# Performance work log

Measured on AMD Instinct MI355X. Metric: run time of the kernel, lower is better.

Reference implementation:

```python
import jax, jax.numpy as jnp
import numpy as np

D_MODEL = 1024
N_HEADS = 16
HEAD_DIM = D_MODEL // N_HEADS
WINDOW = 256
N_GLOBAL = 2
EPS = 1e-5


def _layernorm(x, g, b):
    mu = jnp.mean(x, axis=-1, keepdims=True)
    var = jnp.var(x, axis=-1, keepdims=True)
    return (x - mu) * jax.lax.rsqrt(var + EPS) * g + b


def _longformer_mask(T):
    i = jnp.arange(T)[:, None]
    j = jnp.arange(T)[None, :]
    half = WINDOW // 2
    local = (j >= i - half) & (j <= i + half)
    glob = jnp.zeros((T, T), dtype=bool)
    if N_GLOBAL >= 1:
        glob = glob | (i == 0) | (j == 0)
    if N_GLOBAL >= 2 and T > 1:
        glob = glob | (i == T - 1) | (j == T - 1)
    allowed = (local | glob) & (j <= i)  # causal
    neg_inf = jnp.float32(-jnp.inf)
    return jnp.where(allowed, jnp.float32(0.0), neg_inf)[None, None]  # (1,1,T,T)


def setup_inputs() -> dict:
    key = jax.random.key(0)
    ks = jax.random.split(key, 8)
    B, T, D = 2, 2048, D_MODEL
    s = 0.02
    return {
        "x": jax.random.normal(ks[0], (B, T, D), dtype=jnp.float32),
        "ln1_g": jnp.ones((D,), jnp.float32),
        "ln1_b": jnp.zeros((D,), jnp.float32),
        "ln2_g": jnp.ones((D,), jnp.float32),
        "ln2_b": jnp.zeros((D,), jnp.float32),
        "Wq": jax.random.normal(ks[1], (D, D), jnp.float32) * s,
        "Wk": jax.random.normal(ks[2], (D, D), jnp.float32) * s,
        "Wv": jax.random.normal(ks[3], (D, D), jnp.float32) * s,
        "Wo": jax.random.normal(ks[4], (D, D), jnp.float32) * s,
        "bo": jnp.zeros((D,), jnp.float32),
        "W1": jax.random.normal(ks[5], (D, 4 * D), jnp.float32) * s,
        "b1": jnp.zeros((4 * D,), jnp.float32),
        "W2": jax.random.normal(ks[6], (4 * D, D), jnp.float32) * s,
        "b2": jnp.zeros((D,), jnp.float32),
    }


def reference(x, ln1_g, ln1_b, ln2_g, ln2_b, Wq, Wk, Wv, Wo, bo, W1, b1, W2, b2):
    B, T, D = x.shape
    h = _layernorm(x, ln1_g, ln1_b)
    # (B,T,D) -> (B,H,T,hd)
    q = (h @ Wq).reshape(B, T, N_HEADS, HEAD_DIM).transpose(0, 2, 1, 3)
    k = (h @ Wk).reshape(B, T, N_HEADS, HEAD_DIM).transpose(0, 2, 1, 3)
    v = (h @ Wv).reshape(B, T, N_HEADS, HEAD_DIM).transpose(0, 2, 1, 3)
    mask = _longformer_mask(T)
    scores = jnp.einsum("bhqd,bhkd->bhqk", q, k) / np.sqrt(HEAD_DIM) + mask
    attn = jax.nn.softmax(scores, axis=-1)
    out = jnp.einsum("bhqk,bhkd->bhqd", attn, v)
    out = out.transpose(0, 2, 1, 3).reshape(B, T, D)
    x = x + out @ Wo + bo
    h2 = _layernorm(x, ln2_g, ln2_b)
    ffn = jax.nn.gelu(h2 @ W1 + b1, approximate=False) @ W2 + b2
    return x + ffn
```

## Files before the change

### kernel.cpp

```cpp
#include <hip/hip_runtime.h>
#include <cmath>

#define Tseq 2048
#define Dm   1024
#define NHd  16
#define HDim 64
#define Mrows 4096
#define QS   3072
#define PAD  72
#define NSPLIT 16

typedef _Float16 f16;
typedef _Float16 half8 __attribute__((ext_vector_type(8)));
typedef _Float16 half4 __attribute__((ext_vector_type(4)));
typedef float    floatx4 __attribute__((ext_vector_type(4)));

#define ASYNC_COPY16(g, l)                                                       \
  __builtin_amdgcn_global_load_lds((const __attribute__((address_space(1))) void*)(g), \
                                   (__attribute__((address_space(3))) void*)(l), 16, 0, 0)

__device__ __forceinline__ float gelu_f(float v) {
  const float u = 0.7978845608028654f * (v + 0.044715f * v * v * v);
  const float e = __expf(2.0f * u);
  return 0.5f * v * (2.0f - 2.0f / (e + 1.0f));
}

__global__ __launch_bounds__(256) void transp_f16(const float* __restrict__ W,
                                                  f16* __restrict__ Wt, int K, int N) {
  __shared__ float tile[32][33];
  const int n0 = blockIdx.x * 32, k0 = blockIdx.y * 32;
  const int tx = threadIdx.x & 31, ty = threadIdx.x >> 5;
#pragma unroll
  for (int i = 0; i < 32; i += 8)
    tile[ty + i][tx] = W[(size_t)(k0 + ty + i) * N + n0 + tx];
  __syncthreads();
#pragma unroll
  for (int i = 0; i < 32; i += 8)
    Wt[(size_t)(n0 + ty + i) * K + k0 + tx] = (f16)tile[tx][ty + i];
}

__global__ __launch_bounds__(256) void transp_qkv(const float* __restrict__ Wq,
                                                  const float* __restrict__ Wk,
                                                  const float* __restrict__ Wv,
                                                  f16* __restrict__ Wt) {
  __shared__ float tile[32][33];
  const float* W = (blockIdx.z == 0) ? Wq : (blockIdx.z == 1) ? Wk : Wv;
  f16* dst = Wt + (size_t)blockIdx.z * Dm * Dm;
  const int n0 = blockIdx.x * 32, k0 = blockIdx.y * 32;
  const int tx = threadIdx.x & 31, ty = threadIdx.x >> 5;
#pragma unroll
  for (int i = 0; i < 32; i += 8)
    tile[ty + i][tx] = W[(size_t)(k0 + ty + i) * Dm + n0 + tx];
  __syncthreads();
#pragma unroll
  for (int i = 0; i < 32; i += 8)
    dst[(size_t)(n0 + ty + i) * Dm + k0 + tx] = (f16)tile[tx][ty + i];
}

__global__ __launch_bounds__(256) void ln_f16(const float* __restrict__ x,
                                              const float* __restrict__ g,
                                              const float* __restrict__ bb,
                                              f16* __restrict__ out) {
  const int row = blockIdx.x, t = threadIdx.x;
  const float4 v = ((const float4*)(x + (size_t)row * Dm))[t];
  float s  = v.x + v.y + v.z + v.w;
  float ss = v.x * v.x + v.y * v.y + v.z * v.z + v.w * v.w;
#pragma unroll
  for (int m = 32; m >= 1; m >>= 1) { s += __shfl_xor(s, m); ss += __shfl_xor(ss, m); }
  __shared__ float red[8];
  if ((t & 63) == 0) { red[t >> 6] = s; red[4 + (t >> 6)] = ss; }
  __syncthreads();
  const float S  = red[0] + red[1] + red[2] + red[3];
  const float SS = red[4] + red[5] + red[6] + red[7];
  const float mean = S * (1.0f / Dm);
  const float inv  = rsqrtf(SS * (1.0f / Dm) - mean * mean + 1e-5f);
  const float4 gg = ((const float4*)g)[t];
  const float4 bv = ((const float4*)bb)[t];
  half4 o;
  o.x = (f16)(((v.x - mean) * inv) * gg.x + bv.x);
  o.y = (f16)(((v.y - mean) * inv) * gg.y + bv.y);
  o.z = (f16)(((v.z - mean) * inv) * gg.z + bv.z);
  o.w = (f16)(((v.w - mean) * inv) * gg.w + bv.w);
  *((half4*)(out + (size_t)row * Dm) + t) = o;
}

template <int NS>
__global__ __launch_bounds__(256) void reduce_ln(const f16* __restrict__ P,
                                                 const float* __restrict__ resid,
                                                 const float* __restrict__ bias,
                                                 const float* __restrict__ g,
                                                 const float* __restrict__ bb,
                                                 float* __restrict__ x1,
                                                 f16* __restrict__ h) {
  const int row = blockIdx.x, t = threadIdx.x;
  const size_t idx = (size_t)row * (Dm / 4) + t;
  const float4 r = ((const float4*)resid)[idx];
  const float4 b = ((const float4*)bias)[t];
  float4 o; o.x = r.x + b.x; o.y = r.y + b.y; o.z = r.z + b.z; o.w = r.w + b.w;
#pragma unroll
  for (int z = 0; z < NS; ++z) {
    const half4 p = ((const half4*)(P + (size_t)z * Mrows * Dm))[idx];
    o.x += (float)p[0]; o.y += (float)p[1]; o.z += (float)p[2]; o.w += (float)p[3];
  }
  ((float4*)x1)[idx] = o;
  float s  = o.x + o.y + o.z + o.w;
  float ss = o.x * o.x + o.y * o.y + o.z * o.z + o.w * o.w;
#pragma unroll
  for (int m = 32; m >= 1; m >>= 1) { s += __shfl_xor(s, m); ss += __shfl_xor(ss, m); }
  __shared__ float red[8];
  if ((t & 63) == 0) { red[t >> 6] = s; red[4 + (t >> 6)] = ss; }
  __syncthreads();
  const float S  = red[0] + red[1] + red[2] + red[3];
  const float SS = red[4] + red[5] + red[6] + red[7];
  const float mean = S * (1.0f / Dm);
  const float inv  = rsqrtf(SS * (1.0f / Dm) - mean * mean + 1e-5f);
  const float4 gg = ((const float4*)g)[t];
  const float4 bv = ((const float4*)bb)[t];
  half4 oh;
  oh[0] = (f16)(((o.x - mean) * inv) * gg.x + bv.x);
  oh[1] = (f16)(((o.y - mean) * inv) * gg.y + bv.y);
  oh[2] = (f16)(((o.z - mean) * inv) * gg.z + bv.z);
  oh[3] = (f16)(((o.w - mean) * inv) * gg.w + bv.w);
  ((half4*)h)[idx] = oh;
}

template <int NS>
__global__ __launch_bounds__(256) void reduceK(const f16* __restrict__ P,
                                               const float* __restrict__ resid,
                                               const float* __restrict__ bias,
                                               float* __restrict__ out) {
  const int t = blockIdx.x * 256 + threadIdx.x;
  const int col4 = t & (Dm / 4 - 1);
  const float4 r = ((const float4*)resid)[t];
  const float4 b = ((const float4*)bias)[col4];
  float4 o; o.x = r.x + b.x; o.y = r.y + b.y; o.z = r.z + b.z; o.w = r.w + b.w;
#pragma unroll
  for (int z = 0; z < NS; ++z) {
    const half4 p = ((const half4*)(P + (size_t)z * Mrows * Dm))[t];
    o.x += (float)p[0]; o.y += (float)p[1]; o.z += (float)p[2]; o.w += (float)p[3];
  }
  ((float4*)out)[t] = o;
}

template <int EPI, int LNZ>
__global__ __launch_bounds__(256, 4) void gemm_f16(const f16* __restrict__ A,
                                                   const f16* __restrict__ Bt,
                                                   int M, int N, int K, int kLen,
                                                   const float* __restrict__ bias,
                                                   f16* __restrict__ Ch) {
  constexpr int NZ = 1 << LNZ;
  __shared__ f16 As[128 * 64];
  __shared__ f16 Bs[128 * 64];
  const int tid = threadIdx.x;
  int bx, by, bz;
  if (EPI == 5) {
    const int lin = blockIdx.x;
    bz = lin & (NZ - 1);
    bx = (lin >> LNZ) & 7;
    by = lin >> (LNZ + 3);
  } else {
    bx = blockIdx.x; by = blockIdx.y; bz = 0;
  }
  const int m0 = by * 128, n0 = bx * 128;
  const int kOff = bz * kLen;
  const int w = tid >> 6, l = tid & 63;
  const int wr = (w >> 1) * 64, wc = (w & 1) * 64;
  const int c = l & 15, qq = l >> 4;
  const int cx = c & 7;
  const int srow = tid >> 3;
  const int scol = ((tid & 7) ^ (srow & 7)) * 8;

  floatx4 acc[4][4] = {};

  const f16* Ab = A + (size_t)(m0 + srow) * K + kOff + scol;
  const f16* Bb = Bt + (size_t)(n0 + srow) * K + kOff + scol;

  for (int k0 = 0; k0 < kLen; k0 += 64) {
    __syncthreads();
#pragma unroll
    for (int i = 0; i < 4; ++i) {
      ASYNC_COPY16(Ab + k0 + (size_t)(i * 32) * K, As + i * 2048 + w * 512);
      ASYNC_COPY16(Bb + k0 + (size_t)(i * 32) * K, Bs + i * 2048 + w * 512);
    }
    __syncthreads();
    half8 af[4][2], bfr[4][2];
#pragma unroll
    for (int t = 0; t < 4; ++t) {
      const int ra = (wr + t * 16 + c) * 64;
      af[t][0] = *(const half8*)&As[ra + ((qq ^ cx) * 8)];
      af[t][1] = *(const half8*)&As[ra + (((4 + qq) ^ cx) * 8)];
      const int rb = (wc + t * 16 + c) * 64;
      bfr[t][0] = *(const half8*)&Bs[rb + ((qq ^ cx) * 8)];
      bfr[t][1] = *(const half8*)&Bs[rb + (((4 + qq) ^ cx) * 8)];
    }
#pragma unroll
    for (int ti = 0; ti < 4; ++ti)
#pragma unroll
      for (int tj = 0; tj < 4; ++tj) {
        acc[ti][tj] = __builtin_amdgcn_mfma_f32_16x16x32_f16(af[ti][0], bfr[tj][0], acc[ti][tj], 0, 0, 0);
        acc[ti][tj] = __builtin_amdgcn_mfma_f32_16x16x32_f16(af[ti][1], bfr[tj][1], acc[ti][tj], 0, 0, 0);
      }
  }

  f16* Cw = (EPI == 5) ? (Ch + (size_t)bz * M * N) : Ch;
#pragma unroll
  for (int ti = 0; ti < 4; ++ti)
#pragma unroll
    for (int tj = 0; tj < 4; ++tj)
#pragma unroll
      for (int r = 0; r < 4; ++r) {
        const int row = m0 + wr + ti * 16 + qq * 4 + r;
        const int col = n0 + wc + tj * 16 + c;
        const size_t idx = (size_t)row * N + col;
        float v = acc[ti][tj][r];
        if (EPI == 2) {
          Cw[idx] = (f16)gelu_f(v + bias[col]);
        } else {
          Cw[idx] = (f16)v;
        }
      }
}

__global__ __launch_bounds__(256, 4) void attn_win(const f16* __restrict__ qkv,
                                                   f16* __restrict__ ao) {
  __shared__ f16 qs[64 * PAD];
  __shared__ f16 ks[64 * PAD];
  __shared__ f16 vts[64 * PAD];
  __shared__ f16 ps[64 * PAD];
  const int qt = blockIdx.x;
  const int b = blockIdx.y >> 4, hh = blockIdx.y & 15;
  const int q0 = qt * 64;
  const int tid = threadIdx.x, w = tid >> 6, l = tid & 63;
  const int c = l & 15, qq = l >> 4;
  const int wr = w * 16;
  const size_t base = ((size_t)b * Tseq) * QS + hh * HDim;
  const int rr = tid >> 2, ss = (tid & 3) * 16;

  {
    const f16* src = qkv + base + (size_t)(q0 + rr) * QS + ss;
    *(uint4*)&qs[rr * PAD + ss]     = *(const uint4*)src;
    *(uint4*)&qs[rr * PAD + ss + 8] = *(const uint4*)(src + 8);
  }

  float m_run[4], l_run[4];
  floatx4 oacc[4];
#pragma unroll
  for (int r = 0; r < 4; ++r) { m_run[r] = -INFINITY; l_run[r] = 0.f; }
#pragma unroll
  for (int td = 0; td < 4; ++td) oacc[td] = (floatx4){0.f, 0.f, 0.f, 0.f};

  int chunks[4]; int nch = 0;
  if (qt > 2) chunks[nch++] = 0;
  for (int ch = (qt - 2 > 0 ? qt - 2 : 0); ch <= qt; ++ch) chunks[nch++] = ch;

  for (int ci = 0; ci < nch; ++ci) {
    const int j0 = chunks[ci] * 64;
    __syncthreads();
    {
      const f16* srck = qkv + base + 1024 + (size_t)(j0 + rr) * QS + ss;
      *(uint4*)&ks[rr * PAD + ss]     = *(const uint4*)srck;
      *(uint4*)&ks[rr * PAD + ss + 8] = *(const uint4*)(srck + 8);
      const f16* srcv = qkv + base + 2048 + (size_t)(j0 + rr) * QS + ss;
      uint4 va0 = *(const uint4*)srcv;
      uint4 va1 = *(const uint4*)(srcv + 8);
      const f16* e0 = (const f16*)&va0;
      const f16* e1 = (const f16*)&va1;
#pragma unroll
      for (int i = 0; i < 8; ++i) vts[(ss + i) * PAD + rr] = e0[i];
#pragma unroll
      for (int i = 0; i < 8; ++i) vts[(ss + 8 + i) * PAD + rr] = e1[i];
    }
    __syncthreads();

    const half8 a0 = *(const half8*)&qs[(wr + c) * PAD + qq * 8];
    const half8 a1 = *(const half8*)&qs[(wr + c) * PAD + 32 + qq * 8];
    floatx4 sacc[4];
#pragma unroll
    for (int tj = 0; tj < 4; ++tj) {
      const half8 b0 = *(const half8*)&ks[(tj * 16 + c) * PAD + qq * 8];
      const half8 b1 = *(const half8*)&ks[(tj * 16 + c) * PAD + 32 + qq * 8];
      floatx4 s4 = {0.f, 0.f, 0.f, 0.f};
      s4 = __builtin_amdgcn_mfma_f32_16x16x32_f16(a0, b0, s4, 0, 0, 0);
      s4 = __builtin_amdgcn_mfma_f32_16x16x32_f16(a1, b1, s4, 0, 0, 0);
      sacc[tj] = s4;
    }

#pragma unroll
    for (int r = 0; r < 4; ++r) {
      const int ii = q0 + wr + qq * 4 + r;
      float sv[4];
      float mx = -INFINITY;
#pragma unroll
      for (int tj = 0; tj < 4; ++tj) {
        const int jj = j0 + tj * 16 + c;
        const bool allowed = (jj <= ii) && ((ii - jj) <= 128 || jj == 0);
        sv[tj] = allowed ? sacc[tj][r] * 0.125f : -INFINITY;
        mx = fmaxf(mx, sv[tj]);
      }
#pragma unroll
      for (int mm = 8; mm >= 1; mm >>= 1) mx = fmaxf(mx, __shfl_xor(mx, mm));
      const float mn = fmaxf(m_run[r], mx);
      const float alpha = (mn == -INFINITY) ? 1.f : __expf(m_run[r] - mn);
      float sum = 0.f;
      float p[4];
#pragma unroll
      for (int tj = 0; tj < 4; ++tj) { p[tj] = __expf(sv[tj] - mn); sum += p[tj]; }
#pragma unroll
      for (int mm = 8; mm >= 1; mm >>= 1) sum += __shfl_xor(sum, mm);
      l_run[r] = l_run[r] * alpha + sum;
      m_run[r] = mn;
#pragma unroll
      for (int td = 0; td < 4; ++td) oacc[td][r] *= alpha;
#pragma unroll
      for (int tj = 0; tj < 4; ++tj)
        ps[(wr + qq * 4 + r) * PAD + tj * 16 + c] = (f16)p[tj];
    }

    const half8 p0 = *(const half8*)&ps[(wr + c) * PAD + qq * 8];
    const half8 p1 = *(const half8*)&ps[(wr + c) * PAD + 32 + qq * 8];
#pragma unroll
    for (int td = 0; td < 4; ++td) {
      const half8 b0 = *(const half8*)&vts[(td * 16 + c) * PAD + qq * 8];
      const half8 b1 = *(const half8*)&vts[(td * 16 + c) * PAD + 32 + qq * 8];
      oacc[td] = __builtin_amdgcn_mfma_f32_16x16x32_f16(p0, b0, oacc[td], 0, 0, 0);
      oacc[td] = __builtin_amdgcn_mfma_f32_16x16x32_f16(p1, b1, oacc[td], 0, 0, 0);
    }
  }

#pragma unroll
  for (int td = 0; td < 4; ++td)
#pragma unroll
    for (int r = 0; r < 4; ++r) {
      const int ii = q0 + wr + qq * 4 + r;
      ao[((size_t)(b * Tseq + ii)) * Dm + hh * HDim + td * 16 + c] =
          (f16)(oacc[td][r] / l_run[r]);
    }
}

__global__ __launch_bounds__(256) void attn_row_part(const f16* __restrict__ qkv,
                                                     float* __restrict__ part) {
  const int bh = blockIdx.x, sp = blockIdx.y;
  const int b = bh >> 4, hh = bh & 15;
  const int tid = threadIdx.x;
  const size_t base = ((size_t)b * Tseq) * QS + hh * HDim;
  const int j0 = sp * (Tseq / NSPLIT);
  __shared__ float qsh[64];
  __shared__ float ps[128];
  __shared__ float red[4];
  __shared__ float red2[4];
  __shared__ float oacc[4][64];
  if (tid < 64) qsh[tid] = (float)qkv[base + (size_t)(Tseq - 1) * QS + tid] * 0.125f;
  __syncthreads();
  float sv = -INFINITY;
  if (tid < 128) {
    const f16* kr = qkv + base + 1024 + (size_t)(j0 + tid) * QS;
    float a0 = 0.f;
#pragma unroll
    for (int d8 = 0; d8 < 8; ++d8) {
      const half8 kv = *(const half8*)(kr + d8 * 8);
#pragma unroll
      for (int e = 0; e < 8; ++e) a0 = fmaf((float)kv[e], qsh[d8 * 8 + e], a0);
    }
    sv = a0;
  }
  float mx = sv;
#pragma unroll
  for (int mm = 32; mm >= 1; mm >>= 1) mx = fmaxf(mx, __shfl_xor(mx, mm));
  if ((tid & 63) == 0) red[tid >> 6] = mx;
  __syncthreads();
  const float M = fmaxf(red[0], red[1]);
  float p = 0.f;
  if (tid < 128) { p = __expf(sv - M); ps[tid] = p; }
  float sum = p;
#pragma unroll
  for (int mm = 32; mm >= 1; mm >>= 1) sum += __shfl_xor(sum, mm);
  if ((tid & 63) == 0) red2[tid >> 6] = sum;
  __syncthreads();
  const float L = red2[0] + red2[1];
  const int d = tid & 63, pt = tid >> 6;
  const f16* vb = qkv + base + 2048 + d;
  float acc = 0.f;
  for (int j = pt * 32; j < pt * 32 + 32; ++j)
    acc = fmaf(ps[j], (float)vb[(size_t)(j0 + j) * QS], acc);
  oacc[pt][d] = acc;
  __syncthreads();
  if (tid < 64) {
    const float o = oacc[0][tid] + oacc[1][tid] + oacc[2][tid] + oacc[3][tid];
    float* dst = part + ((size_t)bh * NSPLIT + sp) * 66;
    dst[tid] = o;
    if (tid == 0) { dst[64] = M; dst[65] = L; }
  }
}

__global__ __launch_bounds__(64) void attn_row_comb(const float* __restrict__ part,
                                                    f16* __restrict__ ao) {
  const int bh = blockIdx.x;
  const int b = bh >> 4, hh = bh & 15;
  const int tid = threadIdx.x;
  const float* pp = part + (size_t)bh * NSPLIT * 66;
  float M = -INFINITY;
#pragma unroll
  for (int s = 0; s < NSPLIT; ++s) M = fmaxf(M, pp[s * 66 + 64]);
  float L = 0.f, o = 0.f;
#pragma unroll
  for (int s = 0; s < NSPLIT; ++s) {
    const float wgt = __expf(pp[s * 66 + 64] - M);
    L += pp[s * 66 + 65] * wgt;
    o += pp[s * 66 + tid] * wgt;
  }
  ao[((size_t)(b * Tseq + Tseq - 1)) * Dm + hh * HDim + tid] = (f16)(o / L);
}

extern "C" void kernel_launch(void* const* d_in, const int* in_sizes, int n_in,
                              void* d_out, int out_size, void* d_ws, size_t ws_size,
                              hipStream_t stream) {
  (void)in_sizes; (void)n_in; (void)out_size; (void)ws_size;
  const float* x    = (const float*)d_in[0];
  const float* ln1g = (const float*)d_in[1];
  const float* ln1b = (const float*)d_in[2];
  const float* ln2g = (const float*)d_in[3];
  const float* ln2b = (const float*)d_in[4];
  const float* Wq   = (const float*)d_in[5];
  const float* Wk   = (const float*)d_in[6];
  const float* Wv   = (const float*)d_in[7];
  const float* Wo   = (const float*)d_in[8];
  const float* bo   = (const float*)d_in[9];
  const float* W1   = (const float*)d_in[10];
  const float* b1   = (const float*)d_in[11];
  const float* W2   = (const float*)d_in[12];
  const float* b2   = (const float*)d_in[13];
  float* out = (float*)d_out;

  char* w0 = (char*)d_ws;
  size_t off = 0;
  auto take = [&](size_t bytes) -> char* {
    char* p = w0 + off;
    off += (bytes + 255) & ~(size_t)255;
    return p;
  };
  f16*   WqkvT = (f16*)take((size_t)3 * Dm * Dm * 2);
  f16*   WoT   = (f16*)take((size_t)Dm * Dm * 2);
  f16*   W1T   = (f16*)take((size_t)Dm * 4 * Dm * 2);
  f16*   W2T   = (f16*)take((size_t)Dm * 4 * Dm * 2);
  f16*   hF    = (f16*)take((size_t)Mrows * Dm * 2);
  f16*   qkvh  = (f16*)take((size_t)Mrows * QS * 2);
  f16*   attnF = (f16*)take((size_t)Mrows * Dm * 2);
  float* x1    = (float*)take((size_t)Mrows * Dm * 4);
  f16*   h2F   = (f16*)take((size_t)Mrows * Dm * 2);
  f16*   pbuf  = (f16*)take((size_t)4 * Mrows * Dm * 2);
  float* rowp  = (float*)take((size_t)32 * NSPLIT * 66 * 4);
  f16*   ffn1F = qkvh;

  const dim3 blk(256);
  transp_qkv<<<dim3(Dm / 32, Dm / 32, 3), blk, 0, stream>>>(Wq, Wk, Wv, WqkvT);
  transp_f16<<<dim3(Dm / 32, Dm / 32), blk, 0, stream>>>(Wo, WoT, Dm, Dm);
  transp_f16<<<dim3(4 * Dm / 32, Dm / 32), blk, 0, stream>>>(W1, W1T, Dm, 4 * Dm);
  transp_f16<<<dim3(Dm / 32, 4 * Dm / 32), blk, 0, stream>>>(W2, W2T, 4 * Dm, Dm);

  ln_f16<<<Mrows, blk, 0, stream>>>(x, ln1g, ln1b, hF);

  gemm_f16<3, 0><<<dim3(QS / 128, Mrows / 128), blk, 0, stream>>>(
      hF, WqkvT, Mrows, QS, Dm, Dm, nullptr, qkvh);

  attn_row_part<<<dim3(2 * NHd, NSPLIT), blk, 0, stream>>>(qkvh, rowp);
  attn_win<<<dim3(Tseq / 64, 2 * NHd), blk, 0, stream>>>(qkvh, attnF);
  attn_row_comb<<<dim3(2 * NHd), dim3(64), 0, stream>>>(rowp, attnF);

  gemm_f16<5, 1><<<dim3(512), blk, 0, stream>>>(
      attnF, WoT, Mrows, Dm, Dm, Dm / 2, nullptr, pbuf);
  reduce_ln<2><<<Mrows, blk, 0, stream>>>(pbuf, x, bo, ln2g, ln2b, x1, h2F);

  gemm_f16<2, 0><<<dim3(4 * Dm / 128, Mrows / 128), blk, 0, stream>>>(
      h2F, W1T, Mrows, 4 * Dm, Dm, Dm, b1, ffn1F);

  gemm_f16<5, 2><<<dim3(1024), blk, 0, stream>>>(
      ffn1F, W2T, Mrows, Dm, 4 * Dm, Dm, nullptr, pbuf);
  reduceK<4><<<Mrows * Dm / 1024, blk, 0, stream>>>(pbuf, x1, b2, out);
}
```

Before: 333.6 us.

## Add 256x256 tiled 8-wave GEMM with interleaved async LDS loads and XCD remap

Introduces a new GEMM kernel with 256x256 output tiles, 512 threads and double-buffered LDS fed by async global-to-LDS copies. The copies are interleaved with MFMA phases, and s_setprio is used around the MFMA bursts. Workgroups are remapped across XCDs to improve L2 locality. It replaces the 128x128 GEMM for the QKV projection, FFN1 and split-K FFN2, aiming for more operand reuse per tile. In exchange, fewer workgroups are launched (192 for QKV, 256 for FFN1/FFN2), which may underfill the 256 CUs, and register pressure is high.

```diff
diff --git a/kernel.cpp b/kernel.cpp
--- a/kernel.cpp
+++ b/kernel.cpp
@@ -18,6 +18,13 @@
 #define ASYNC_COPY16(g, l)                                                       \
   __builtin_amdgcn_global_load_lds((const __attribute__((address_space(1))) void*)(g), \
                                    (__attribute__((address_space(3))) void*)(l), 16, 0, 0)
+
+#define SBAR()                                    \
+  do {                                            \
+    asm volatile("" ::: "memory");                \
+    __builtin_amdgcn_s_barrier();                 \
+    asm volatile("" ::: "memory");                \
+  } while (0)
 
 __device__ __forceinline__ float gelu_f(float v) {
   const float u = 0.7978845608028654f * (v + 0.044715f * v * v * v);
@@ -219,6 +226,167 @@
           Cw[idx] = (f16)v;
         }
       }
+}
+
+template <int EPI, int LNZ, int NT>
+__global__ __launch_bounds__(512, 2) void gemm256(const f16* __restrict__ A,
+                                                  const f16* __restrict__ Bt,
+                                                  int M, int N, int Kd,
+                                                  const float* __restrict__ bias,
+                                                  f16* __restrict__ Ch) {
+  __shared__ f16 As[2][256 * 64];
+  __shared__ f16 Bs[2][256 * 64];
+
+  const int nwg = gridDim.x;
+  const int lin = blockIdx.x;
+  const int q8 = nwg >> 3, r8 = nwg & 7;
+  const int xcd = lin & 7, idx8 = lin >> 3;
+  const int wgid = (xcd < r8 ? xcd * (q8 + 1) : r8 * (q8 + 1) + (xcd - r8) * q8) + idx8;
+  int bz = 0, rest = wgid;
+  if (EPI == 5) {
+    const int zLen = nwg >> LNZ;
+    bz = wgid / zLen;
+    rest = wgid - bz * zLen;
+  }
+  const int nbx = N >> 8;
+  const int bx = rest % nbx, by = rest / nbx;
+  const int m0 = by << 8, n0 = bx << 8;
+  const int kOff = bz * (NT * 64);
+
+  const int tid = threadIdx.x;
+  const int w = tid >> 6, l = tid & 63;
+  const int c = l & 15, qq = l >> 4, cx = c & 7;
+  const int wr = (w >> 2) << 7;
+  const int wc = (w & 3) << 6;
+  const int srow = tid >> 3;
+  const int scol = ((tid & 7) ^ (srow & 7)) << 3;
+
+  const f16* gA = A + (size_t)(m0 + srow) * Kd + kOff + scol;
+  const f16* gB = Bt + (size_t)(n0 + srow) * Kd + kOff + scol;
+  const int ldsW = (w << 3) * 64;
+
+  floatx4 acc[8][4] = {};
+
+  {
+    ASYNC_COPY16(gA,                         &As[0][ldsW]);
+    ASYNC_COPY16(gA + (size_t)64 * Kd,       &As[0][ldsW + 64 * 64]);
+    ASYNC_COPY16(gA + (size_t)128 * Kd,      &As[0][(128 << 6) + ldsW]);
+    ASYNC_COPY16(gA + (size_t)192 * Kd,      &As[0][(192 << 6) + ldsW]);
+    ASYNC_COPY16(gB,                         &Bs[0][ldsW]);
+    ASYNC_COPY16(gB + (size_t)64 * Kd,       &Bs[0][ldsW + 64 * 64]);
+    ASYNC_COPY16(gB + (size_t)128 * Kd,      &Bs[0][(128 << 6) + ldsW]);
+    ASYNC_COPY16(gB + (size_t)192 * Kd,      &Bs[0][(192 << 6) + ldsW]);
+    ASYNC_COPY16(gA + 64,                    &As[1][ldsW]);
+    ASYNC_COPY16(gA + 64 + (size_t)64 * Kd,  &As[1][ldsW + 64 * 64]);
+    ASYNC_COPY16(gA + 64 + (size_t)128 * Kd, &As[1][(128 << 6) + ldsW]);
+    ASYNC_COPY16(gA + 64 + (size_t)192 * Kd, &As[1][(192 << 6) + ldsW]);
+    asm volatile("s_waitcnt vmcnt(4)" ::: "memory");
+    SBAR();
+  }
+
+  half8 a0[8], a1[8], b0[4], b1[4];
+
+#pragma unroll 2
+  for (int t = 0; t < NT; ++t) {
+    const int cur = t & 1;
+    const f16* Ab = As[cur];
+    const f16* Bb = Bs[cur];
+
+    if (t + 1 < NT) {
+      const f16* g = gB + (size_t)(t + 1) * 64;
+      ASYNC_COPY16(g,                   &Bs[cur ^ 1][ldsW]);
+      ASYNC_COPY16(g + (size_t)64 * Kd, &Bs[cur ^ 1][ldsW + 64 * 64]);
+    }
+#pragma unroll
+    for (int mq = 0; mq < 8; ++mq)
+      a0[mq] = *(const half8*)&Ab[(wr + mq * 16 + c) * 64 + ((qq ^ cx) << 3)];
+#pragma unroll
+    for (int nq = 0; nq < 4; ++nq)
+      b0[nq] = *(const half8*)&Bb[(wc + nq * 16 + c) * 64 + ((qq ^ cx) << 3)];
+    SBAR();
+    __builtin_amdgcn_s_setprio(1);
+#pragma unroll
+    for (int mq = 0; mq < 4; ++mq)
+#pragma unroll
+      for (int nq = 0; nq < 4; ++nq)
+        acc[mq][nq] = __builtin_amdgcn_mfma_f32_16x16x32_f16(a0[mq], b0[nq], acc[mq][nq], 0, 0, 0);
+    __builtin_amdgcn_s_setprio(0);
+    SBAR();
+
+    if (t + 1 < NT) {
+      const f16* g = gB + (size_t)(t + 1) * 64 + (size_t)128 * Kd;
+      ASYNC_COPY16(g,                   &Bs[cur ^ 1][(128 << 6) + ldsW]);
+      ASYNC_COPY16(g + (size_t)64 * Kd, &Bs[cur ^ 1][(192 << 6) + ldsW]);
+    }
+#pragma unroll
+    for (int mq = 0; mq < 8; ++mq)
+      a1[mq] = *(const half8*)&Ab[(wr + mq * 16 + c) * 64 + (((4 + qq) ^ cx) << 3)];
+#pragma unroll
+    for (int nq = 0; nq < 4; ++nq)
+      b1[nq] = *(const half8*)&Bb[(wc + nq * 16 + c) * 64 + (((4 + qq) ^ cx) << 3)];
+    SBAR();
+    __builtin_amdgcn_s_setprio(1);
+#pragma unroll
+    for (int mq = 4; mq < 8; ++mq)
+#pragma unroll
+      for (int nq = 0; nq < 4; ++nq)
+        acc[mq][nq] = __builtin_amdgcn_mfma_f32_16x16x32_f16(a0[mq], b0[nq], acc[mq][nq], 0, 0, 0);
+    __builtin_amdgcn_s_setprio(0);
+    asm volatile("s_waitcnt lgkmcnt(0)" ::: "memory");
+    SBAR();
+
+    if (t + 2 < NT) {
+      const f16* g = gA + (size_t)(t + 2) * 64;
+      ASYNC_COPY16(g,                   &As[cur][ldsW]);
+      ASYNC_COPY16(g + (size_t)64 * Kd, &As[cur][ldsW + 64 * 64]);
+    }
+    SBAR();
+    __builtin_amdgcn_s_setprio(1);
+#pragma unroll
+    for (int mq = 0; mq < 4; ++mq)
+#pragma unroll
+      for (int nq = 0; nq < 4; ++nq)
+        acc[mq][nq] = __builtin_amdgcn_mfma_f32_16x16x32_f16(a1[mq], b1[nq], acc[mq][nq], 0, 0, 0);
+    __builtin_amdgcn_s_setprio(0);
+    SBAR();
+
+    if (t + 2 < NT) {
+      const f16* g = gA + (size_t)(t + 2) * 64 + (size_t)128 * Kd;
+      ASYNC_COPY16(g,                   &As[cur][(128 << 6) + ldsW]);
+      ASYNC_COPY16(g + (size_t)64 * Kd, &As[cur][(192 << 6) + ldsW]);
+    }
+    SBAR();
+    __builtin_amdgcn_s_setprio(1);
+#pragma unroll
+    for (int mq = 4; mq < 8; ++mq)
+#pragma unroll
+      for (int nq = 0; nq < 4; ++nq)
+        acc[mq][nq] = __builtin_amdgcn_mfma_f32_16x16x32_f16(a1[mq], b1[nq], acc[mq][nq], 0, 0, 0);
+    __builtin_amdgcn_s_setprio(0);
+    if (t < NT - 2) asm volatile("s_waitcnt vmcnt(4)" ::: "memory");
+    else            asm volatile("s_waitcnt vmcnt(0)" ::: "memory");
+    SBAR();
+  }
+
+  float bias_v[4] = {0.f, 0.f, 0.f, 0.f};
+  if (EPI == 2) {
+#pragma unroll
+    for (int nq = 0; nq < 4; ++nq) bias_v[nq] = bias[n0 + wc + nq * 16 + c];
+  }
+  f16* Cw = (EPI == 5) ? (Ch + (size_t)bz * M * N) : Ch;
+#pragma unroll
+  for (int mq = 0; mq < 8; ++mq)
+#pragma unroll
+    for (int r = 0; r < 4; ++r) {
+      const size_t rowb = (size_t)(m0 + wr + mq * 16 + qq * 4 + r) * N;
+#pragma unroll
+      for (int nq = 0; nq < 4; ++nq) {
+        const int col = n0 + wc + nq * 16 + c;
+        const float v = acc[mq][nq][r];
+        if (EPI == 2) Cw[rowb + col] = (f16)gelu_f(v + bias_v[nq]);
+        else          Cw[rowb + col] = (f16)v;
+      }
+    }
 }
 
 __global__ __launch_bounds__(256, 4) void attn_win(const f16* __restrict__ qkv,
@@ -452,6 +620,7 @@
   f16*   ffn1F = qkvh;
 
   const dim3 blk(256);
+  const dim3 blk512(512);
   transp_qkv<<<dim3(Dm / 32, Dm / 32, 3), blk, 0, stream>>>(Wq, Wk, Wv, WqkvT);
   transp_f16<<<dim3(Dm / 32, Dm / 32), blk, 0, stream>>>(Wo, WoT, Dm, Dm);
   transp_f16<<<dim3(4 * Dm / 32, Dm / 32), blk, 0, stream>>>(W1, W1T, Dm, 4 * Dm);
@@ -459,8 +628,8 @@
 
   ln_f16<<<Mrows, blk, 0, stream>>>(x, ln1g, ln1b, hF);
 
-  gemm_f16<3, 0><<<dim3(QS / 128, Mrows / 128), blk, 0, stream>>>(
-      hF, WqkvT, Mrows, QS, Dm, Dm, nullptr, qkvh);
+  gemm256<3, 0, 16><<<dim3((Mrows / 256) * (QS / 256)), blk512, 0, stream>>>(
+      hF, WqkvT, Mrows, QS, Dm, nullptr, qkvh);
 
   attn_row_part<<<dim3(2 * NHd, NSPLIT), blk, 0, stream>>>(qkvh, rowp);
   attn_win<<<dim3(Tseq / 64, 2 * NHd), blk, 0, stream>>>(qkvh, attnF);
@@ -470,10 +639,10 @@
       attnF, WoT, Mrows, Dm, Dm, Dm / 2, nullptr, pbuf);
   reduce_ln<2><<<Mrows, blk, 0, stream>>>(pbuf, x, bo, ln2g, ln2b, x1, h2F);
 
-  gemm_f16<2, 0><<<dim3(4 * Dm / 128, Mrows / 128), blk, 0, stream>>>(
-      h2F, W1T, Mrows, 4 * Dm, Dm, Dm, b1, ffn1F);
-
-  gemm_f16<5, 2><<<dim3(1024), blk, 0, stream>>>(
-      ffn1F, W2T, Mrows, Dm, 4 * Dm, Dm, nullptr, pbuf);
+  gemm256<2, 0, 16><<<dim3((Mrows / 256) * (4 * Dm / 256)), blk512, 0, stream>>>(
+      h2F, W1T, Mrows, 4 * Dm, Dm, b1, ffn1F);
+
+  gemm256<5, 2, 16><<<dim3(4 * (Mrows / 256) * (Dm / 256)), blk512, 0, stream>>>(
+      ffn1F, W2T, Mrows, Dm, 4 * Dm, nullptr, pbuf);
   reduceK<4><<<Mrows * Dm / 1024, blk, 0, stream>>>(pbuf, x1, b2, out);
 }
```

Measured after the change: 425.0 us. 27.4% more time.

## Merge prep and attention kernels into single launches and add XCD-aware GEMM tile mapping

Applied to the files above, without the earlier changes.

The four weight-transpose kernels and the first layernorm are combined into one `prep` launch that dispatches on a linear block index. The global-row partial-attention kernel is folded into the windowed-attention kernel as extra blocks, reusing its shared memory, so both run in one launch. Non-split GEMMs now map their 1D block index so that each XCD receives a contiguous group of N-tiles, aiming for better L2 reuse of weight tiles. This cuts launch overhead and lets independent work overlap, at the cost of more branching in the kernels and a heterogeneous block mix.

```diff
diff --git a/kernel.cpp b/kernel.cpp
--- a/kernel.cpp
+++ b/kernel.cpp
@@ -25,10 +25,10 @@
   return 0.5f * v * (2.0f - 2.0f / (e + 1.0f));
 }
 
-__global__ __launch_bounds__(256) void transp_f16(const float* __restrict__ W,
-                                                  f16* __restrict__ Wt, int K, int N) {
-  __shared__ float tile[32][33];
-  const int n0 = blockIdx.x * 32, k0 = blockIdx.y * 32;
+__device__ __forceinline__ void transp_body(const float* __restrict__ W,
+                                            f16* __restrict__ Wt, int K, int N,
+                                            int bx, int by, float (*tile)[33]) {
+  const int n0 = bx * 32, k0 = by * 32;
   const int tx = threadIdx.x & 31, ty = threadIdx.x >> 5;
 #pragma unroll
   for (int i = 0; i < 32; i += 8)
@@ -39,35 +39,46 @@
     Wt[(size_t)(n0 + ty + i) * K + k0 + tx] = (f16)tile[tx][ty + i];
 }
 
-__global__ __launch_bounds__(256) void transp_qkv(const float* __restrict__ Wq,
-                                                  const float* __restrict__ Wk,
-                                                  const float* __restrict__ Wv,
-                                                  f16* __restrict__ Wt) {
+__global__ __launch_bounds__(256) void prep(const float* __restrict__ Wq,
+                                            const float* __restrict__ Wk,
+                                            const float* __restrict__ Wv,
+                                            const float* __restrict__ Wo,
+                                            const float* __restrict__ W1,
+                                            const float* __restrict__ W2,
+                                            const float* __restrict__ x,
+                                            const float* __restrict__ g,
+                                            const float* __restrict__ bb,
+                                            f16* __restrict__ WqkvT,
+                                            f16* __restrict__ WoT,
+                                            f16* __restrict__ W1T,
+                                            f16* __restrict__ W2T,
+                                            f16* __restrict__ hF) {
   __shared__ float tile[32][33];
-  const float* W = (blockIdx.z == 0) ? Wq : (blockIdx.z == 1) ? Wk : Wv;
-  f16* dst = Wt + (size_t)blockIdx.z * Dm * Dm;
-  const int n0 = blockIdx.x * 32, k0 = blockIdx.y * 32;
-  const int tx = threadIdx.x & 31, ty = threadIdx.x >> 5;
-#pragma unroll
-  for (int i = 0; i < 32; i += 8)
-    tile[ty + i][tx] = W[(size_t)(k0 + ty + i) * Dm + n0 + tx];
-  __syncthreads();
-#pragma unroll
-  for (int i = 0; i < 32; i += 8)
-    dst[(size_t)(n0 + ty + i) * Dm + k0 + tx] = (f16)tile[tx][ty + i];
-}
-
-__global__ __launch_bounds__(256) void ln_f16(const float* __restrict__ x,
-                                              const float* __restrict__ g,
-                                              const float* __restrict__ bb,
-                                              f16* __restrict__ out) {
-  const int row = blockIdx.x, t = threadIdx.x;
+  __shared__ float red[8];
+  const int lin = blockIdx.x;
+  if (lin < 4096) {
+    const int wsel = lin >> 10, t = lin & 1023;
+    const float* W = (wsel == 0) ? Wq : (wsel == 1) ? Wk : (wsel == 2) ? Wv : Wo;
+    f16* dst = (wsel < 3) ? (WqkvT + (size_t)wsel * Dm * Dm) : WoT;
+    transp_body(W, dst, Dm, Dm, t & 31, t >> 5, tile);
+    return;
+  }
+  if (lin < 8192) {
+    const int t = lin - 4096;
+    transp_body(W1, W1T, Dm, 4 * Dm, t & 127, t >> 7, tile);
+    return;
+  }
+  if (lin < 12288) {
+    const int t = lin - 8192;
+    transp_body(W2, W2T, 4 * Dm, Dm, t & 31, t >> 5, tile);
+    return;
+  }
+  const int row = lin - 12288, t = threadIdx.x;
   const float4 v = ((const float4*)(x + (size_t)row * Dm))[t];
   float s  = v.x + v.y + v.z + v.w;
   float ss = v.x * v.x + v.y * v.y + v.z * v.z + v.w * v.w;
 #pragma unroll
   for (int m = 32; m >= 1; m >>= 1) { s += __shfl_xor(s, m); ss += __shfl_xor(ss, m); }
-  __shared__ float red[8];
   if ((t & 63) == 0) { red[t >> 6] = s; red[4 + (t >> 6)] = ss; }
   __syncthreads();
   const float S  = red[0] + red[1] + red[2] + red[3];
@@ -81,7 +92,7 @@
   o.y = (f16)(((v.y - mean) * inv) * gg.y + bv.y);
   o.z = (f16)(((v.z - mean) * inv) * gg.z + bv.z);
   o.w = (f16)(((v.w - mean) * inv) * gg.w + bv.w);
-  *((half4*)(out + (size_t)row * Dm) + t) = o;
+  *((half4*)(hF + (size_t)row * Dm) + t) = o;
 }
 
 template <int NS>
@@ -159,7 +170,11 @@
     bx = (lin >> LNZ) & 7;
     by = lin >> (LNZ + 3);
   } else {
-    bx = blockIdx.x; by = blockIdx.y; bz = 0;
+    const int nbx = N >> 7, chunk = nbx >> 3;
+    const int xcd = blockIdx.x & 7, idx = blockIdx.x >> 3;
+    bx = xcd * chunk + idx % chunk;
+    by = idx / chunk;
+    bz = 0;
   }
   const int m0 = by * 128, n0 = bx * 128;
   const int kOff = bz * kLen;
@@ -221,16 +236,76 @@
       }
 }
 
-__global__ __launch_bounds__(256, 4) void attn_win(const f16* __restrict__ qkv,
-                                                   f16* __restrict__ ao) {
+__global__ __launch_bounds__(256, 4) void attn_fused(const f16* __restrict__ qkv,
+                                                     f16* __restrict__ ao,
+                                                     float* __restrict__ part) {
   __shared__ f16 qs[64 * PAD];
   __shared__ f16 ks[64 * PAD];
   __shared__ f16 vts[64 * PAD];
   __shared__ f16 ps[64 * PAD];
-  const int qt = blockIdx.x;
-  const int b = blockIdx.y >> 4, hh = blockIdx.y & 15;
+  const int lin = blockIdx.x;
+  const int tid = threadIdx.x;
+
+  if (lin >= 1024) {
+    const int r_ = lin - 1024;
+    const int bh = r_ & 31, sp = r_ >> 5;
+    const int b = bh >> 4, hh = bh & 15;
+    const size_t base = ((size_t)b * Tseq) * QS + hh * HDim;
+    const int j0 = sp * (Tseq / NSPLIT);
+    float* qsh  = (float*)qs;
+    float* psf  = (float*)ks;
+    float* red  = (float*)vts;
+    float* red2 = red + 4;
+    float (*oaccp)[64] = (float(*)[64])ps;
+    if (tid < 64) qsh[tid] = (float)qkv[base + (size_t)(Tseq - 1) * QS + tid] * 0.125f;
+    __syncthreads();
+    float sv = -INFINITY;
+    if (tid < 128) {
+      const f16* kr = qkv + base + 1024 + (size_t)(j0 + tid) * QS;
+      float a0 = 0.f;
+#pragma unroll
+      for (int d8 = 0; d8 < 8; ++d8) {
+        const half8 kv = *(const half8*)(kr + d8 * 8);
+#pragma unroll
+        for (int e = 0; e < 8; ++e) a0 = fmaf((float)kv[e], qsh[d8 * 8 + e], a0);
+      }
+      sv = a0;
+    }
+    float mx = sv;
+#pragma unroll
+    for (int mm = 32; mm >= 1; mm >>= 1) mx = fmaxf(mx, __shfl_xor(mx, mm));
+    if ((tid & 63) == 0) red[tid >> 6] = mx;
+    __syncthreads();
+    const float M = fmaxf(red[0], red[1]);
+    float p = 0.f;
+    if (tid < 128) { p = __expf(sv - M); psf[tid] = p; }
+    float sum = p;
+#pragma unroll
+    for (int mm = 32; mm >= 1; mm >>= 1) sum += __shfl_xor(sum, mm);
+    if ((tid & 63) == 0) red2[tid >> 6] = sum;
+    __syncthreads();
+    const float L = red2[0] + red2[1];
+    const int d = tid & 63, pt = tid >> 6;
+    const f16* vb = qkv + base + 2048 + d;
+    float acc = 0.f;
+    for (int j = pt * 32; j < pt * 32 + 32; ++j)
+      acc = fmaf(psf[j], (float)vb[(size_t)(j0 + j) * QS], acc);
+    oaccp[pt][d] = acc;
+    __syncthreads();
+    if (tid < 64) {
+      const float o = oaccp[0][tid] + oaccp[1][tid] + oaccp[2][tid] + oaccp[3][tid];
+      float* dst = part + ((size_t)bh * NSPLIT + sp) * 66;
+      dst[tid] = o;
+      if (tid == 0) { dst[64] = M; dst[65] = L; }
+    }
+    return;
+  }
+
+  const int qt = lin & 31;
+  const int byv = lin >> 5;
+  const int b = byv >> 4, hh = byv & 15;
   const int q0 = qt * 64;
-  const int tid = threadIdx.x, w = tid >> 6, l = tid & 63;
+  const int w = tid >> 6, l = tid & 63;
   const int c = l & 15, qq = l >> 4;
   const int wr = w * 16;
   const size_t base = ((size_t)b * Tseq) * QS + hh * HDim;
@@ -335,61 +410,6 @@
       ao[((size_t)(b * Tseq + ii)) * Dm + hh * HDim + td * 16 + c] =
           (f16)(oacc[td][r] / l_run[r]);
     }
-}
-
-__global__ __launch_bounds__(256) void attn_row_part(const f16* __restrict__ qkv,
-                                                     float* __restrict__ part) {
-  const int bh = blockIdx.x, sp = blockIdx.y;
-  const int b = bh >> 4, hh = bh & 15;
-  const int tid = threadIdx.x;
-  const size_t base = ((size_t)b * Tseq) * QS + hh * HDim;
-  const int j0 = sp * (Tseq / NSPLIT);
-  __shared__ float qsh[64];
-  __shared__ float ps[128];
-  __shared__ float red[4];
-  __shared__ float red2[4];
-  __shared__ float oacc[4][64];
-  if (tid < 64) qsh[tid] = (float)qkv[base + (size_t)(Tseq - 1) * QS + tid] * 0.125f;
-  __syncthreads();
-  float sv = -INFINITY;
-  if (tid < 128) {
-    const f16* kr = qkv + base + 1024 + (size_t)(j0 + tid) * QS;
-    float a0 = 0.f;
-#pragma unroll
-    for (int d8 = 0; d8 < 8; ++d8) {
-      const half8 kv = *(const half8*)(kr + d8 * 8);
-#pragma unroll
-      for (int e = 0; e < 8; ++e) a0 = fmaf((float)kv[e], qsh[d8 * 8 + e], a0);
-    }
-    sv = a0;
-  }
-  float mx = sv;
-#pragma unroll
-  for (int mm = 32; mm >= 1; mm >>= 1) mx = fmaxf(mx, __shfl_xor(mx, mm));
-  if ((tid & 63) == 0) red[tid >> 6] = mx;
-  __syncthreads();
-  const float M = fmaxf(red[0], red[1]);
-  float p = 0.f;
-  if (tid < 128) { p = __expf(sv - M); ps[tid] = p; }
-  float sum = p;
-#pragma unroll
-  for (int mm = 32; mm >= 1; mm >>= 1) sum += __shfl_xor(sum, mm);
-  if ((tid & 63) == 0) red2[tid >> 6] = sum;
-  __syncthreads();
-  const float L = red2[0] + red2[1];
-  const int d = tid & 63, pt = tid >> 6;
-  const f16* vb = qkv + base + 2048 + d;
-  float acc = 0.f;
-  for (int j = pt * 32; j < pt * 32 + 32; ++j)
-    acc = fmaf(ps[j], (float)vb[(size_t)(j0 + j) * QS], acc);
-  oacc[pt][d] = acc;
-  __syncthreads();
-  if (tid < 64) {
-    const float o = oacc[0][tid] + oacc[1][tid] + oacc[2][tid] + oacc[3][tid];
-    float* dst = part + ((size_t)bh * NSPLIT + sp) * 66;
-    dst[tid] = o;
-    if (tid == 0) { dst[64] = M; dst[65] = L; }
-  }
 }
 
 __global__ __launch_bounds__(64) void attn_row_comb(const float* __restrict__ part,
@@ -452,25 +472,21 @@
   f16*   ffn1F = qkvh;
 
   const dim3 blk(256);
-  transp_qkv<<<dim3(Dm / 32, Dm / 32, 3), blk, 0, stream>>>(Wq, Wk, Wv, WqkvT);
-  transp_f16<<<dim3(Dm / 32, Dm / 32), blk, 0, stream>>>(Wo, WoT, Dm, Dm);
-  transp_f16<<<dim3(4 * Dm / 32, Dm / 32), blk, 0, stream>>>(W1, W1T, Dm, 4 * Dm);
-  transp_f16<<<dim3(Dm / 32, 4 * Dm / 32), blk, 0, stream>>>(W2, W2T, 4 * Dm, Dm);
-
-  ln_f16<<<Mrows, blk, 0, stream>>>(x, ln1g, ln1b, hF);
-
-  gemm_f16<3, 0><<<dim3(QS / 128, Mrows / 128), blk, 0, stream>>>(
+
+  prep<<<dim3(16384), blk, 0, stream>>>(Wq, Wk, Wv, Wo, W1, W2, x, ln1g, ln1b,
+                                        WqkvT, WoT, W1T, W2T, hF);
+
+  gemm_f16<3, 0><<<dim3(768), blk, 0, stream>>>(
       hF, WqkvT, Mrows, QS, Dm, Dm, nullptr, qkvh);
 
-  attn_row_part<<<dim3(2 * NHd, NSPLIT), blk, 0, stream>>>(qkvh, rowp);
-  attn_win<<<dim3(Tseq / 64, 2 * NHd), blk, 0, stream>>>(qkvh, attnF);
+  attn_fused<<<dim3(1536), blk, 0, stream>>>(qkvh, attnF, rowp);
   attn_row_comb<<<dim3(2 * NHd), dim3(64), 0, stream>>>(rowp, attnF);
 
   gemm_f16<5, 1><<<dim3(512), blk, 0, stream>>>(
       attnF, WoT, Mrows, Dm, Dm, Dm / 2, nullptr, pbuf);
   reduce_ln<2><<<Mrows, blk, 0, stream>>>(pbuf, x, bo, ln2g, ln2b, x1, h2F);
 
-  gemm_f16<2, 0><<<dim3(4 * Dm / 128, Mrows / 128), blk, 0, stream>>>(
+  gemm_f16<2, 0><<<dim3(1024), blk, 0, stream>>>(
       h2F, W1T, Mrows, 4 * Dm, Dm, Dm, b1, ffn1F);
 
   gemm_f16<5, 2><<<dim3(1024), blk, 0, stream>>>(
```

Measured after the change: 314.9 us. 1.06x faster.
